# Kernel optimization log

Measured on AMD Instinct MI355X. Metric: run time of the kernel, lower is better.

The kernel has to match this reference:

```python
import jax, jax.numpy as jnp
import numpy as np

NDIM = 1024
NTOKEN = 50257
CUTOFFS = [2000, 10000, NTOKEN]  # cutoffs + [ntoken]
DIV = 4
N = 4096
HEAD_SIZE = CUTOFFS[0] + len(CUTOFFS) - 1  # 2002


def setup_inputs() -> dict:
    key = jax.random.key(0)
    ks = jax.random.split(key, 8)
    inputs = jax.random.normal(ks[0], (N, NDIM), dtype=jnp.float32)
    targets = jax.random.randint(ks[1], (N,), 0, NTOKEN, dtype=jnp.int32)
    # head: nn.Linear(ndim, head_size, bias=False) -> weight [head_size, ndim], xavier
    def xavier(k, shape):
        fan_out, fan_in = shape
        lim = np.sqrt(6.0 / (fan_in + fan_out))
        return jax.random.uniform(k, shape, jnp.float32, -lim, lim)
    head_W = xavier(ks[2], (HEAD_SIZE, NDIM))
    # tail cluster 0: size 8000, low dim 256; cluster 1: size 40257, low dim 64
    sz0 = CUTOFFS[1] - CUTOFFS[0]
    sz1 = CUTOFFS[2] - CUTOFFS[1]
    d0, d1 = NDIM // DIV, NDIM // DIV**2
    emb0 = jax.random.normal(ks[3], (sz0, d0), dtype=jnp.float32) * d0 ** -0.5
    emb1 = jax.random.normal(ks[4], (sz1, d1), dtype=jnp.float32) * d1 ** -0.5
    lin0 = xavier(ks[5], (NDIM, d0))  # nn.Linear(d0, ndim).weight
    lin1 = xavier(ks[6], (NDIM, d1))
    return {"inputs": inputs, "targets": targets, "head_W": head_W,
            "emb0": emb0, "lin0": lin0, "emb1": emb1, "lin1": lin1}


def _adaptive_logprob(inputs, targets, head_W, emb0, lin0, emb1, lin1):
    tails = [(emb0, lin0), (emb1, lin1)]
    # map targets -> head targets (in-head id, or cluster slot cutoffs[0]+i)
    head_targets = targets
    masks = []
    for i in range(len(tails)):
        m = (targets >= CUTOFFS[i]) & (targets < CUTOFFS[i + 1])
        masks.append(m)
        head_targets = jnp.where(m, CUTOFFS[0] + i, head_targets)
    # head: logits [N, head_size], gather per-row log-prob
    head_lp = jax.nn.log_softmax(inputs @ head_W.T, axis=-1)
    out = jnp.take_along_axis(head_lp, head_targets[:, None], axis=1)[:, 0]
    # tails: logits = (x @ lin) @ emb^T (low-rank), log-softmax, masked gather
    for i, (emb, lin) in enumerate(tails):
        size = CUTOFFS[i + 1] - CUTOFFS[i]
        lp = jax.nn.log_softmax((inputs @ lin) @ emb.T, axis=-1)  # [N, size]
        rel = jnp.clip(targets - CUTOFFS[i], 0, size - 1)
        g = jnp.take_along_axis(lp, rel[:, None], axis=1)[:, 0]
        out = out + jnp.where(masks[i], g, 0.0)
    return out


def reference(inputs, targets, head_W, emb0, lin0, emb1, lin1):
    outputs = _adaptive_logprob(inputs, targets, head_W, emb0, lin0, emb1, lin1)
    loss = (-outputs).mean()
    return outputs, loss
```

## Files before the change

### kernel.cpp

```cpp
#include <hip/hip_runtime.h>


typedef __attribute__((ext_vector_type(8))) short short8;
typedef __attribute__((ext_vector_type(4))) float f32x4;

#define LOG2E 1.4426950408889634f
#define LN2   0.6931471805599453f

__device__ __forceinline__ float b2f(unsigned short u){
    return __uint_as_float(((unsigned int)u) << 16);
}
__device__ __forceinline__ unsigned short f2b(float f){
    unsigned int x = __float_as_uint(f);
    x += 0x7fffu + ((x >> 16) & 1u);
    return (unsigned short)(x >> 16);
}
__device__ __forceinline__ float dotu(unsigned int xu, unsigned int wu){
    float a = __uint_as_float(xu << 16) * __uint_as_float(wu << 16);
    float b = __uint_as_float(xu & 0xffff0000u) * __uint_as_float(wu & 0xffff0000u);
    return a + b;
}
__device__ __forceinline__ float fexp2(float x){
#if __has_builtin(__builtin_amdgcn_exp2f)
    return __builtin_amdgcn_exp2f(x);
#else
    float r; asm("v_exp_f32 %0, %1" : "=v"(r) : "v"(x)); return r;
#endif
}
__device__ __forceinline__ void gload16(const unsigned short* g, unsigned short* l){
    __builtin_amdgcn_global_load_lds(
        (const __attribute__((address_space(1))) unsigned int*)g,
        (__attribute__((address_space(3))) unsigned int*)l, 16, 0, 0);
}

__global__ __launch_bounds__(256) void k_prep(
    const float* __restrict__ X, const float* __restrict__ headW,
    const float* __restrict__ emb0, const float* __restrict__ emb1,
    const float* __restrict__ lin0, const float* __restrict__ lin1,
    const int* __restrict__ tgt,
    unsigned short* __restrict__ Xb, unsigned short* __restrict__ hWb,
    unsigned short* __restrict__ e0b, unsigned short* __restrict__ e1b,
    unsigned short* __restrict__ l0T, unsigned short* __restrict__ l1T,
    int* __restrict__ idx0, int* __restrict__ idx1,
    int* __restrict__ pos0, int* __restrict__ pos1, int* __restrict__ cnt)
{
    __shared__ unsigned short tileT[64][65];
    const int b = blockIdx.x, t = threadIdx.x;
    if (b < 80){
        const float* src; unsigned short* dst; int C, tx, ty;
        if (b < 64){ src = lin0; dst = l0T; C = 256; tx = b & 3; ty = b >> 2; }
        else       { src = lin1; dst = l1T; C = 64;  tx = 0;     ty = b - 64; }
        #pragma unroll
        for (int e = 0; e < 16; ++e){
            int idx = t + e*256, r = idx >> 6, c = idx & 63;
            tileT[c][r] = f2b(src[(ty*64 + r)*C + tx*64 + c]);
        }
        __syncthreads();
        #pragma unroll
        for (int e = 0; e < 16; ++e){
            int idx = t + e*256, cc = idx >> 6, rr = idx & 63;
            dst[(tx*64 + cc)*1024 + ty*64 + rr] = tileT[cc][rr];
        }
        return;
    }
    const int NX = 1048576, NH = 512512, NE0 = 512000, NE1 = 644112;
    const int NV = NX + NH + NE0 + NE1;
    const int total = NV + 4096;
    int stride = (gridDim.x - 80) * 256;
    for (int i = (b - 80)*256 + t; i < total; i += stride){
        if (i < NV){
            const float* src; unsigned short* dst; int off; float sc;
            if (i < NX)            { src = X;     dst = Xb;  off = i;           sc = 1.0f;  }
            else if (i < NX+NH)    { src = headW; dst = hWb; off = i-NX;        sc = LOG2E; }
            else if (i < NX+NH+NE0){ src = emb0;  dst = e0b; off = i-NX-NH;     sc = LOG2E; }
            else                   { src = emb1;  dst = e1b; off = i-NX-NH-NE0; sc = LOG2E; }
            float4 v = ((const float4*)src)[off];
            ushort4 o;
            o.x = f2b(v.x*sc); o.y = f2b(v.y*sc);
            o.z = f2b(v.z*sc); o.w = f2b(v.w*sc);
            ((ushort4*)dst)[off] = o;
        } else {
            int row = i - NV;
            int tv = tgt[row];
            int p0 = 0, p1 = 0;
            if (tv >= 2000 && tv < 10000){
                int p = atomicAdd(&cnt[0], 1); idx0[p] = row; p0 = p;
            } else if (tv >= 10000){
                int p = atomicAdd(&cnt[1], 1); idx1[p] = row; p1 = p;
            }
            pos0[row] = p0; pos1[row] = p1;
        }
    }
}

__global__ __launch_bounds__(256) void k_hgemm(
    const unsigned short* __restrict__ A,
    const unsigned short* __restrict__ B0, unsigned short* __restrict__ C0,
    const unsigned short* __restrict__ B1, unsigned short* __restrict__ C1,
    const int* __restrict__ idx0, const int* __restrict__ idx1,
    const int* __restrict__ cnt)
{
    constexpr int K = 1024;
    __shared__ __align__(16) unsigned short As[64*64];
    __shared__ __align__(16) unsigned short Bs[64*64];

    const int j = blockIdx.x;
    const bool isH0 = (j < 256);
    const int band = isH0 ? (j >> 2) : (j - 256);
    const int cntv = isH0 ? cnt[0] : cnt[1];
    if (band >= ((cntv + 63) >> 6)) return;
    const unsigned short* B = isH0 ? B0 : B1;
    unsigned short* C = isH0 ? C0 : C1;
    const int M  = isH0 ? 256 : 64;
    const int cb = isH0 ? (j & 3) : 0;
    const int* idx = isH0 ? idx0 : idx1;

    const int tid  = threadIdx.x;
    const int lane = tid & 63;
    const int w    = tid >> 6;
    const int waveR = w >> 1, waveC = w & 1;
    const int quad  = lane >> 4, l16 = lane & 15;

    const int r0l = tid >> 3, r1l = r0l + 32, g = tid & 7;
    const int gr0 = idx[min(band*64 + r0l, cntv - 1)];
    const int gr1 = idx[min(band*64 + r1l, cntv - 1)];

    f32x4 acc[2][2];
    #pragma unroll
    for (int i = 0; i < 2; ++i)
    #pragma unroll
    for (int jj = 0; jj < 2; ++jj) acc[i][jj] = (f32x4){0.f,0.f,0.f,0.f};

    for (int kc = 0; kc < K/64; ++kc){
        __syncthreads();
        *((uint4*)&As[r0l*64 + ((g ^ (r0l & 7)) << 3)]) =
            *(const uint4*)(A + (size_t)gr0*K + kc*64 + g*8);
        *((uint4*)&As[r1l*64 + ((g ^ (r1l & 7)) << 3)]) =
            *(const uint4*)(A + (size_t)gr1*K + kc*64 + g*8);
        *((uint4*)&Bs[r0l*64 + ((g ^ (r0l & 7)) << 3)]) =
            *(const uint4*)(B + (size_t)(cb*64 + r0l)*K + kc*64 + g*8);
        *((uint4*)&Bs[r1l*64 + ((g ^ (r1l & 7)) << 3)]) =
            *(const uint4*)(B + (size_t)(cb*64 + r1l)*K + kc*64 + g*8);
        __syncthreads();
        #pragma unroll
        for (int ks = 0; ks < 2; ++ks){
            short8 a[2], bb[2];
            #pragma unroll
            for (int i = 0; i < 2; ++i){
                int r = waveR*32 + i*16 + l16;
                int gg = ks*4 + quad;
                a[i] = *(const short8*)&As[r*64 + ((gg ^ (r & 7)) << 3)];
            }
            #pragma unroll
            for (int jj = 0; jj < 2; ++jj){
                int r = waveC*32 + jj*16 + l16;
                int gg = ks*4 + quad;
                bb[jj] = *(const short8*)&Bs[r*64 + ((gg ^ (r & 7)) << 3)];
            }
            #pragma unroll
            for (int i = 0; i < 2; ++i)
            #pragma unroll
            for (int jj = 0; jj < 2; ++jj)
                acc[i][jj] = __builtin_amdgcn_mfma_f32_16x16x32_bf16(
                    a[i], bb[jj], acc[i][jj], 0, 0, 0);
        }
    }
    #pragma unroll
    for (int i = 0; i < 2; ++i)
    #pragma unroll
    for (int jj = 0; jj < 2; ++jj)
    #pragma unroll
    for (int r = 0; r < 4; ++r){
        int crow = band*64 + waveR*32 + i*16 + quad*4 + r;
        int col  = cb*64 + waveC*32 + jj*16 + l16;
        C[crow*M + col] = f2b(acc[i][jj][r]);
    }
}

template<int K>
__device__ __forceinline__ void sumexp_lds(
    const unsigned short* __restrict__ A,
    const unsigned short* __restrict__ B,
    float* __restrict__ s_out, int M,
    int rowb, int cb0, int cb1,
    unsigned short* __restrict__ As, unsigned short* __restrict__ Bs,
    const int* __restrict__ idx, int cnt)
{
    constexpr int KCH = K / 64;
    constexpr int LK  = (KCH == 16) ? 4 : 2;
    static_assert(KCH == 16 || KCH == 4, "");
    const int tid  = threadIdx.x;
    const int lane = tid & 63, w = tid >> 6;
    const int waveR = w >> 1, waveC = w & 1;
    const int quad  = lane >> 4, l16 = lane & 15;
    const int row0  = rowb * 64;
    const int nit   = (cb1 - cb0) << LK;

    float s_loc[8];
    #pragma unroll
    for (int i = 0; i < 8; ++i) s_loc[i] = 0.f;
    f32x4 acc[2][2];
    #pragma unroll
    for (int i = 0; i < 2; ++i)
    #pragma unroll
    for (int j = 0; j < 2; ++j) acc[i][j] = (f32x4){0.f,0.f,0.f,0.f};

    const int sr = w*16 + (lane >> 3);
    const int gk = ((lane & 7) ^ (sr & 7)) << 3;

    int aoff[2][2], boff[2][2];
    #pragma unroll
    for (int x = 0; x < 2; ++x)
    #pragma unroll
    for (int ks = 0; ks < 2; ++ks){
        int ra = waveR*32 + x*16 + l16;
        int rb = waveC*32 + x*16 + l16;
        int g  = ks*4 + quad;
        aoff[x][ks] = ra*64 + ((g ^ (ra & 7)) << 3);
        boff[x][ks] = rb*64 + ((g ^ (rb & 7)) << 3);
    }

    auto stage = [&](int it){
        int cb = cb0 + (it >> LK);
        int kc = it & (KCH - 1);
        unsigned short* Ad = As + (it & 1)*4096 + w*1024;
        unsigned short* Bd = Bs + (it & 1)*4096 + w*1024;
        const unsigned short* ga = A + (size_t)(row0 + sr)*K + kc*64 + gk;
        gload16(ga,        Ad);
        gload16(ga + 8*K,  Ad + 512);
        int br0 = cb*64 + sr;     if (br0 > M-1) br0 = M-1;
        int br1 = cb*64 + sr + 8; if (br1 > M-1) br1 = M-1;
        gload16(B + (size_t)br0*K + kc*64 + gk, Bd);
        gload16(B + (size_t)br1*K + kc*64 + gk, Bd + 512);
    };

    stage(0);
    __syncthreads();

    for (int it = 0; it < nit; ++it){
        if (it + 1 < nit) stage(it + 1);
        const unsigned short* Ac = As + (it & 1)*4096;
        const unsigned short* Bc = Bs + (it & 1)*4096;
        #pragma unroll
        for (int ks = 0; ks < 2; ++ks){
            short8 a0 = *(const short8*)(Ac + aoff[0][ks]);
            short8 a1 = *(const short8*)(Ac + aoff[1][ks]);
            short8 b0 = *(const short8*)(Bc + boff[0][ks]);
            short8 b1 = *(const short8*)(Bc + boff[1][ks]);
            acc[0][0] = __builtin_amdgcn_mfma_f32_16x16x32_bf16(a0, b0, acc[0][0], 0,0,0);
            acc[0][1] = __builtin_amdgcn_mfma_f32_16x16x32_bf16(a0, b1, acc[0][1], 0,0,0);
            acc[1][0] = __builtin_amdgcn_mfma_f32_16x16x32_bf16(a1, b0, acc[1][0], 0,0,0);
            acc[1][1] = __builtin_amdgcn_mfma_f32_16x16x32_bf16(a1, b1, acc[1][1], 0,0,0);
        }
        if ((it & (KCH - 1)) == (KCH - 1)){
            int cb = cb0 + (it >> LK);
            if ((cb + 1)*64 <= M){
                #pragma unroll
                for (int i = 0; i < 2; ++i)
                #pragma unroll
                for (int j = 0; j < 2; ++j)
                #pragma unroll
                for (int r = 0; r < 4; ++r)
                    s_loc[i*4 + r] += fexp2(acc[i][j][r]);
            } else {
                #pragma unroll
                for (int j = 0; j < 2; ++j){
                    int col = cb*64 + waveC*32 + j*16 + l16;
                    if (col < M){
                        #pragma unroll
                        for (int i = 0; i < 2; ++i)
                        #pragma unroll
                        for (int r = 0; r < 4; ++r)
                            s_loc[i*4 + r] += fexp2(acc[i][j][r]);
                    }
                }
            }
            #pragma unroll
            for (int i = 0; i < 2; ++i)
            #pragma unroll
            for (int j = 0; j < 2; ++j) acc[i][j] = (f32x4){0.f,0.f,0.f,0.f};
        }
        __syncthreads();
    }

    #pragma unroll
    for (int k = 0; k < 8; ++k){
        #pragma unroll
        for (int m = 1; m < 16; m <<= 1)
            s_loc[k] += __shfl_xor(s_loc[k], m, 64);
    }
    if (l16 < 8){
        int i = l16 >> 2, r = l16 & 3;
        int lrow = row0 + waveR*32 + i*16 + quad*4 + r;
        if (idx){
            if (lrow < cnt) atomicAdd(&s_out[idx[lrow]], s_loc[l16]);
        } else {
            atomicAdd(&s_out[lrow], s_loc[l16]);
        }
    }
}

__device__ __forceinline__ void sumexp_stream64(
    const unsigned short* __restrict__ A,
    const unsigned short* __restrict__ B,
    float* __restrict__ s_out, int row0, int g0, int g1,
    const int* __restrict__ idx, int cnt)
{
    const int M = 40257;
    const int lane = threadIdx.x & 63;
    const int quad = lane >> 4, l16 = lane & 15;

    short8 a[4][2];
    #pragma unroll
    for (int i = 0; i < 4; ++i)
    #pragma unroll
    for (int ks = 0; ks < 2; ++ks)
        a[i][ks] = *(const short8*)(A + (size_t)(row0 + i*16 + l16)*64 + ks*32 + quad*8);

    f32x4 sums[4];
    #pragma unroll
    for (int i = 0; i < 4; ++i) sums[i] = (f32x4){0.f,0.f,0.f,0.f};

    short8 p0a, p1a, p0b, p1b;
    auto loadB = [&](int g, short8& d0, short8& d1){
        int n = g*16 + l16; if (n > M-1) n = M-1;
        const unsigned short* p = B + (size_t)n*64 + quad*8;
        d0 = *(const short8*)p;
        d1 = *(const short8*)(p + 32);
    };
    auto body = [&](int g, short8 b0, short8 b1){
        f32x4 acc[4];
        #pragma unroll
        for (int i = 0; i < 4; ++i) acc[i] = (f32x4){0.f,0.f,0.f,0.f};
        #pragma unroll
        for (int i = 0; i < 4; ++i)
            acc[i] = __builtin_amdgcn_mfma_f32_16x16x32_bf16(a[i][0], b0, acc[i], 0,0,0);
        #pragma unroll
        for (int i = 0; i < 4; ++i)
            acc[i] = __builtin_amdgcn_mfma_f32_16x16x32_bf16(a[i][1], b1, acc[i], 0,0,0);
        if (g*16 + l16 < M){
            #pragma unroll
            for (int i = 0; i < 4; ++i){
                sums[i][0] += fexp2(acc[i][0]);
                sums[i][1] += fexp2(acc[i][1]);
                sums[i][2] += fexp2(acc[i][2]);
                sums[i][3] += fexp2(acc[i][3]);
            }
        }
    };

    loadB(g0, p0a, p1a);
    loadB(g0 + 1, p0b, p1b);
    for (int g = g0; g < g1; g += 2){
        body(g, p0a, p1a);
        if (g + 2 < g1) loadB(g + 2, p0a, p1a);
        if (g + 1 < g1){
            body(g + 1, p0b, p1b);
            if (g + 3 < g1) loadB(g + 3, p0b, p1b);
        }
    }

    #pragma unroll
    for (int i = 0; i < 4; ++i){
        #pragma unroll
        for (int r = 0; r < 4; ++r){
            float v = sums[i][r];
            v += __shfl_xor(v, 1, 64);
            v += __shfl_xor(v, 2, 64);
            v += __shfl_xor(v, 4, 64);
            v += __shfl_xor(v, 8, 64);
            int orow = row0 + i*16 + quad*4 + r;
            if (l16 == 0 && orow < cnt)
                atomicAdd(&s_out[idx[orow]], v);
        }
    }
}

__global__ __launch_bounds__(256) void k_sumexp(
    const unsigned short* __restrict__ Xb,  const unsigned short* __restrict__ hWb,
    const unsigned short* __restrict__ h0b, const unsigned short* __restrict__ e0b,
    const unsigned short* __restrict__ h1b, const unsigned short* __restrict__ e1b,
    float* __restrict__ sH, float* __restrict__ s0, float* __restrict__ s1,
    const int* __restrict__ idx0, const int* __restrict__ idx1,
    const int* __restrict__ cnt)
{
    __shared__ __align__(16) unsigned short As[2*4096];
    __shared__ __align__(16) unsigned short Bs[2*4096];
    const int b = blockIdx.x;
    const int m4 = b & 3;
    if (m4 == 0){
        int id = b >> 2, rowb = id >> 3, split = id & 7;
        sumexp_lds<1024>(Xb, hWb, sH, 2002, rowb, split*4, split*4 + 4,
                         As, Bs, nullptr, 4096);
    } else if (m4 == 2){
        int id = b >> 2, rowb = id >> 3, split = id & 7;
        int c0 = cnt[0];
        if (rowb < ((c0 + 63) >> 6)){
            int cb0 = split*15 + min(split, 5);
            int cb1 = cb0 + 15 + (split < 5 ? 1 : 0);
            sumexp_lds<256>(h0b, e0b, s0, 8000, rowb, cb0, cb1,
                            As, Bs, idx0, c0);
        }
    } else {
        int wid = (b >> 1)*4 + (threadIdx.x >> 6);
        int rowg = wid >> 6, split = wid & 63;
        int c1 = cnt[1];
        if (rowg < ((c1 + 63) >> 6)){
            int g0 = split*39 + min(split, 21);
            int g1 = g0 + 39 + (split < 21 ? 1 : 0);
            sumexp_stream64(h1b, e1b, s1, rowg*64, g0, g1, idx1, c1);
        }
    }
}

__global__ __launch_bounds__(256) void k_combine(
    const unsigned short* __restrict__ Xb,   const unsigned short* __restrict__ hWb,
    const unsigned short* __restrict__ h0b,  const unsigned short* __restrict__ e0b,
    const unsigned short* __restrict__ h1b,  const unsigned short* __restrict__ e1b,
    const float* __restrict__ sH, const float* __restrict__ s0,
    const float* __restrict__ s1,
    const int* __restrict__ targets,
    const int* __restrict__ pos0, const int* __restrict__ pos1,
    float* __restrict__ lossacc, int* __restrict__ ticket,
    float* __restrict__ out)
{
    __shared__ float red4[4];
    int w = threadIdx.x >> 6, lane = threadIdx.x & 63;
    int row = blockIdx.x*4 + w;
    int t = targets[row];
    int hidx = t < 2000 ? t : (t < 10000 ? 2000 : 2001);
    int c0 = pos0[row], c1 = pos1[row];

    float dh = 0.f;
    {
        const uint4* xa = (const uint4*)(Xb  + (size_t)row*1024  + lane*16);
        const uint4* wb = (const uint4*)(hWb + (size_t)hidx*1024 + lane*16);
        #pragma unroll
        for (int p = 0; p < 2; ++p){
            uint4 xv = xa[p], wv = wb[p];
            dh += dotu(xv.x, wv.x) + dotu(xv.y, wv.y)
                + dotu(xv.z, wv.z) + dotu(xv.w, wv.w);
        }
    }
    int rel0 = min(max(t - 2000, 0), 7999);
    int rel1 = min(max(t - 10000, 0), 40256);
    float d0;
    {
        uint2 xv = *(const uint2*)(h0b + (size_t)c0*256  + lane*4);
        uint2 wv = *(const uint2*)(e0b + (size_t)rel0*256 + lane*4);
        d0 = dotu(xv.x, wv.x) + dotu(xv.y, wv.y);
    }
    float d1 = b2f(h1b[(size_t)c1*64 + lane]) * b2f(e1b[(size_t)rel1*64 + lane]);

    #pragma unroll
    for (int m = 1; m < 64; m <<= 1){
        dh += __shfl_xor(dh, m, 64);
        d0 += __shfl_xor(d0, m, 64);
        d1 += __shfl_xor(d1, m, 64);
    }
    if (lane == 0){
        float lp = dh - log2f(sH[row]);
        if (t >= 2000 && t < 10000) lp += d0 - log2f(s0[row]);
        if (t >= 10000)             lp += d1 - log2f(s1[row]);
        float val = LN2 * lp;
        out[row] = val;
        red4[w] = val;
    }
    __syncthreads();
    if (threadIdx.x == 0){
        atomicAdd(lossacc, red4[0] + red4[1] + red4[2] + red4[3]);
        __threadfence();
        int old = atomicAdd(ticket, 1);
        if (old == 1023){
            __threadfence();
            float tot = atomicAdd(lossacc, 0.0f);
            out[4096] = -tot / 4096.f;
        }
    }
}

extern "C" void kernel_launch(void* const* d_in, const int* in_sizes, int n_in,
                              void* d_out, int out_size, void* d_ws, size_t ws_size,
                              hipStream_t stream) {
    const float* X      = (const float*)d_in[0];
    const int*   tgt    = (const int*)  d_in[1];
    const float* headW  = (const float*)d_in[2];
    const float* emb0   = (const float*)d_in[3];
    const float* lin0   = (const float*)d_in[4];
    const float* emb1   = (const float*)d_in[5];
    const float* lin1   = (const float*)d_in[6];
    float* out = (float*)d_out;

    char* ws = (char*)d_ws;
    unsigned short* Xb  = (unsigned short*)(ws + 0);
    unsigned short* hWb = (unsigned short*)(ws + 8388608);
    unsigned short* e0b = (unsigned short*)(ws + 12488704);
    unsigned short* e1b = (unsigned short*)(ws + 16584704);
    unsigned short* l0T = (unsigned short*)(ws + 21737600);
    unsigned short* l1T = (unsigned short*)(ws + 22261888);
    unsigned short* h0b = (unsigned short*)(ws + 22392960);
    unsigned short* h1b = (unsigned short*)(ws + 24490112);
    float* sums         = (float*)(ws + 25014400);
    int*   cnt          = (int*)  (ws + 25063552);
    int*   ticket       = (int*)  (ws + 25063560);
    float* lossacc      = (float*)(ws + 25063564);
    int*   idx0         = (int*)  (ws + 25063568);
    int*   idx1         = (int*)  (ws + 25079952);
    int*   pos0         = (int*)  (ws + 25096336);
    int*   pos1         = (int*)  (ws + 25112720);
    float* sH = sums, *s0 = sums + 4096, *s1 = sums + 8192;

    hipMemsetAsync(ws + 25014400, 0, 49168, stream);

    k_prep<<<2048, 256, 0, stream>>>(X, headW, emb0, emb1, lin0, lin1, tgt,
                                     Xb, hWb, e0b, e1b, l0T, l1T,
                                     idx0, idx1, pos0, pos1, cnt);
    k_hgemm<<<320, 256, 0, stream>>>(Xb, l0T, h0b, l1T, h1b, idx0, idx1, cnt);
    k_sumexp<<<2048, 256, 0, stream>>>(Xb, hWb, h0b, e0b, h1b, e1b,
                                       sH, s0, s1, idx0, idx1, cnt);
    k_combine<<<1024, 256, 0, stream>>>(Xb, hWb, h0b, e0b, h1b, e1b,
                                        sH, s0, s1, tgt, pos0, pos1,
                                        lossacc, ticket, out);
}
```

Before: 243.9 us.

## Replace memset and atomic bucketing with in-kernel scan and remap sumexp blocks

Removes the hipMemsetAsync launch by zeroing sums, ticket and lossacc inside k_prep. Target bucketing now uses a single block with a serial prefix scan instead of per-row global atomics, which gives a deterministic row order. k_sumexp block indices are remapped so the 8 column splits of a row band sit on adjacent block IDs, which may improve L2 reuse of the A tile. The single-thread scan over 256 entries adds a short serial tail to that one block.

```diff
diff --git a/kernel.cpp b/kernel.cpp
--- a/kernel.cpp
+++ b/kernel.cpp
@@ -42,11 +42,13 @@
     unsigned short* __restrict__ e0b, unsigned short* __restrict__ e1b,
     unsigned short* __restrict__ l0T, unsigned short* __restrict__ l1T,
     int* __restrict__ idx0, int* __restrict__ idx1,
-    int* __restrict__ pos0, int* __restrict__ pos1, int* __restrict__ cnt)
+    int* __restrict__ pos0, int* __restrict__ pos1, int* __restrict__ cnt,
+    int* __restrict__ ticket, float* __restrict__ lossacc,
+    float* __restrict__ sums)
 {
-    __shared__ unsigned short tileT[64][65];
     const int b = blockIdx.x, t = threadIdx.x;
     if (b < 80){
+        __shared__ unsigned short tileT[64][65];
         const float* src; unsigned short* dst; int C, tx, ty;
         if (b < 64){ src = lin0; dst = l0T; C = 256; tx = b & 3; ty = b >> 2; }
         else       { src = lin1; dst = l1T; C = 64;  tx = 0;     ty = b - 64; }
@@ -63,11 +65,40 @@
         }
         return;
     }
+    if (b == 80){
+        __shared__ int sc0[257], sc1[257];
+        int tv[16]; int c0 = 0, c1 = 0;
+        #pragma unroll
+        for (int r = 0; r < 16; ++r){
+            int v = tgt[t*16 + r]; tv[r] = v;
+            c0 += (v >= 2000 && v < 10000);
+            c1 += (v >= 10000);
+        }
+        sc0[t+1] = c0; sc1[t+1] = c1;
+        if (t == 0){ sc0[0] = 0; sc1[0] = 0; *ticket = 0; *lossacc = 0.f; }
+        __syncthreads();
+        if (t == 0){
+            for (int i = 1; i <= 256; ++i){ sc0[i] += sc0[i-1]; sc1[i] += sc1[i-1]; }
+            cnt[0] = sc0[256]; cnt[1] = sc1[256];
+        }
+        __syncthreads();
+        int b0 = sc0[t], b1 = sc1[t];
+        #pragma unroll
+        for (int r = 0; r < 16; ++r){
+            int row = t*16 + r, v = tv[r];
+            int p0 = 0, p1 = 0;
+            if (v >= 2000 && v < 10000){ idx0[b0] = row; p0 = b0++; }
+            else if (v >= 10000)       { idx1[b1] = row; p1 = b1++; }
+            pos0[row] = p0; pos1[row] = p1;
+        }
+        return;
+    }
     const int NX = 1048576, NH = 512512, NE0 = 512000, NE1 = 644112;
     const int NV = NX + NH + NE0 + NE1;
-    const int total = NV + 4096;
-    int stride = (gridDim.x - 80) * 256;
-    for (int i = (b - 80)*256 + t; i < total; i += stride){
+    const int NS = 12288;
+    const int total = NV + NS;
+    int stride = (gridDim.x - 81) * 256;
+    for (int i = (b - 81)*256 + t; i < total; i += stride){
         if (i < NV){
             const float* src; unsigned short* dst; int off; float sc;
             if (i < NX)            { src = X;     dst = Xb;  off = i;           sc = 1.0f;  }
@@ -80,15 +111,7 @@
             o.z = f2b(v.z*sc); o.w = f2b(v.w*sc);
             ((ushort4*)dst)[off] = o;
         } else {
-            int row = i - NV;
-            int tv = tgt[row];
-            int p0 = 0, p1 = 0;
-            if (tv >= 2000 && tv < 10000){
-                int p = atomicAdd(&cnt[0], 1); idx0[p] = row; p0 = p;
-            } else if (tv >= 10000){
-                int p = atomicAdd(&cnt[1], 1); idx1[p] = row; p1 = p;
-            }
-            pos0[row] = p0; pos1[row] = p1;
+            sums[i - NV] = 0.f;
         }
     }
 }
@@ -387,23 +410,26 @@
     __shared__ __align__(16) unsigned short As[2*4096];
     __shared__ __align__(16) unsigned short Bs[2*4096];
     const int b = blockIdx.x;
-    const int m4 = b & 3;
-    if (m4 == 0){
-        int id = b >> 2, rowb = id >> 3, split = id & 7;
-        sumexp_lds<1024>(Xb, hWb, sH, 2002, rowb, split*4, split*4 + 4,
+    const int x = b & 7, q = b >> 3;
+    const int qm = q & 3;
+    if (qm == 0){
+        int rowb = q >> 2;
+        sumexp_lds<1024>(Xb, hWb, sH, 2002, rowb, x*4, x*4 + 4,
                          As, Bs, nullptr, 4096);
-    } else if (m4 == 2){
-        int id = b >> 2, rowb = id >> 3, split = id & 7;
+    } else if (qm == 2){
+        int band = q >> 2;
         int c0 = cnt[0];
-        if (rowb < ((c0 + 63) >> 6)){
-            int cb0 = split*15 + min(split, 5);
-            int cb1 = cb0 + 15 + (split < 5 ? 1 : 0);
-            sumexp_lds<256>(h0b, e0b, s0, 8000, rowb, cb0, cb1,
+        if (band < ((c0 + 63) >> 6)){
+            int cb0 = x*15 + min(x, 5);
+            int cb1 = cb0 + 15 + (x < 5 ? 1 : 0);
+            sumexp_lds<256>(h0b, e0b, s0, 8000, band, cb0, cb1,
                             As, Bs, idx0, c0);
         }
     } else {
-        int wid = (b >> 1)*4 + (threadIdx.x >> 6);
-        int rowg = wid >> 6, split = wid & 63;
+        int m = q >> 1;
+        int w4 = threadIdx.x >> 6;
+        int rowg = m >> 1;
+        int split = x*8 + ((m & 1) << 2) + w4;
         int c1 = cnt[1];
         if (rowg < ((c1 + 63) >> 6)){
             int g0 = split*39 + min(split, 21);
@@ -510,11 +536,10 @@
     int*   pos1         = (int*)  (ws + 25112720);
     float* sH = sums, *s0 = sums + 4096, *s1 = sums + 8192;
 
-    hipMemsetAsync(ws + 25014400, 0, 49168, stream);
-
     k_prep<<<2048, 256, 0, stream>>>(X, headW, emb0, emb1, lin0, lin1, tgt,
                                      Xb, hWb, e0b, e1b, l0T, l1T,
-                                     idx0, idx1, pos0, pos1, cnt);
+                                     idx0, idx1, pos0, pos1, cnt,
+                                     ticket, lossacc, sums);
     k_hgemm<<<320, 256, 0, stream>>>(Xb, l0T, h0b, l1T, h1b, idx0, idx1, cnt);
     k_sumexp<<<2048, 256, 0, stream>>>(Xb, hWb, h0b, e0b, h1b, e1b,
                                        sH, s0, s1, idx0, idx1, cnt);
```

New measurement: 253.9 us. +4.1%, slower.
